# Performance work log

Measured on AMD Instinct MI355X. Metric: run time of the kernel, lower is better.

Reference implementation:

```python
import jax, jax.numpy as jnp
import numpy as np

D = 768
NH = 8
HD = D // NH
LAT = 64


def layernorm(x, g, b, eps=1e-5):
    mu = x.mean(-1, keepdims=True)
    var = ((x - mu) ** 2).mean(-1, keepdims=True)
    return (x - mu) * jax.lax.rsqrt(var + eps) * g + b


def mha(q, k, v, qw, qb, kw, kb, vw, vb, ow, ob):
    # torch nn.MultiheadAttention (batch_first): Linear is x @ W.T + b
    B, Lq, _ = q.shape
    qh = (q @ qw.T + qb).reshape(B, Lq, NH, HD)
    kh = (k @ kw.T + kb).reshape(B, -1, NH, HD)
    vh = (v @ vw.T + vb).reshape(B, -1, NH, HD)
    s = jnp.einsum('bqhd,bkhd->bhqk', qh, kh) * (1.0 / np.sqrt(HD))
    a = jax.nn.softmax(s, axis=-1)
    o = jnp.einsum('bhqk,bkhd->bqhd', a, vh).reshape(B, Lq, D)
    return o @ ow.T + ob


def setup_inputs() -> dict:
    key = jax.random.key(0)
    ks = jax.random.split(key, 16)
    w = lambda k, shape: (jax.random.normal(k, shape, jnp.float32) * 0.02)
    inp = {
        'frames': jax.random.normal(ks[0], (4, 4, 8, 3, 224, 224), jnp.float32),
        'pe_w': w(ks[1], (D, 3, 14, 14)), 'pe_b': jnp.zeros((D,), jnp.float32),
        'latents': jax.random.normal(ks[2], (LAT, D), jnp.float32),
        'ca_qw': w(ks[3], (D, D)), 'ca_qb': jnp.zeros((D,), jnp.float32),
        'ca_kw': w(ks[4], (D, D)), 'ca_kb': jnp.zeros((D,), jnp.float32),
        'ca_vw': w(ks[5], (D, D)), 'ca_vb': jnp.zeros((D,), jnp.float32),
        'ca_ow': w(ks[6], (D, D)), 'ca_ob': jnp.zeros((D,), jnp.float32),
        'nq_g': jnp.ones((D,), jnp.float32), 'nq_b': jnp.zeros((D,), jnp.float32),
        'nkv_g': jnp.ones((D,), jnp.float32), 'nkv_b': jnp.zeros((D,), jnp.float32),
        'no_g': jnp.ones((D,), jnp.float32), 'no_b': jnp.zeros((D,), jnp.float32),
        'm1_w': w(ks[7], (4 * D, D)), 'm1_b': jnp.zeros((4 * D,), jnp.float32),
        'm2_w': w(ks[8], (D, 4 * D)), 'm2_b': jnp.zeros((D,), jnp.float32),
        'sa_qw': w(ks[9], (D, D)), 'sa_qb': jnp.zeros((D,), jnp.float32),
        'sa_kw': w(ks[10], (D, D)), 'sa_kb': jnp.zeros((D,), jnp.float32),
        'sa_vw': w(ks[11], (D, D)), 'sa_vb': jnp.zeros((D,), jnp.float32),
        'sa_ow': w(ks[12], (D, D)), 'sa_ob': jnp.zeros((D,), jnp.float32),
        'f1_w': w(ks[13], (2 * D, D)), 'f1_b': jnp.zeros((2 * D,), jnp.float32),
        'f2_w': w(ks[14], (D, 2 * D)), 'f2_b': jnp.zeros((D,), jnp.float32),
        'n1_g': jnp.ones((D,), jnp.float32), 'n1_b': jnp.zeros((D,), jnp.float32),
        'n2_g': jnp.ones((D,), jnp.float32), 'n2_b': jnp.zeros((D,), jnp.float32),
    }
    return inp


def reference(frames, pe_w, pe_b, latents, ca_qw, ca_qb, ca_kw, ca_kb, ca_vw, ca_vb,
              ca_ow, ca_ob, nq_g, nq_b, nkv_g, nkv_b, no_g, no_b, m1_w, m1_b, m2_w, m2_b,
              sa_qw, sa_qb, sa_kw, sa_kb, sa_vw, sa_vb, sa_ow, sa_ob, f1_w, f1_b,
              f2_w, f2_b, n1_g, n1_b, n2_g, n2_b):
    B, S, T, C, H, W = frames.shape
    # --- patch embed (Conv2d k=14 s=14), batched over all seconds & frames ---
    f = frames.reshape(B * S * T, C, H, W)
    p = jax.lax.conv_general_dilated(
        f, pe_w, window_strides=(14, 14), padding='VALID',
        dimension_numbers=('NCHW', 'OIHW', 'NCHW')) + pe_b[None, :, None, None]
    npatch = p.shape[2] * p.shape[3]  # 256 patches per frame
    p = p.reshape(B * S * T, D, npatch).transpose(0, 2, 1)  # [BST, P, D]
    kv = p.reshape(B * S, T * npatch, D)  # per-second patch tokens
    # --- Perceiver second tokenizer (loop over seconds == batched over B*S) ---
    q = jnp.broadcast_to(latents[None], (B * S, LAT, D))
    out = mha(layernorm(q, nq_g, nq_b), layernorm(kv, nkv_g, nkv_b), kv,
              ca_qw, ca_qb, ca_kw, ca_kb, ca_vw, ca_vb, ca_ow, ca_ob)
    h = layernorm(out, no_g, no_b)
    tok = out + (jax.nn.gelu(h @ m1_w.T + m1_b) @ m2_w.T + m2_b)
    # concat second tokens along time
    x = tok.reshape(B, S * LAT, D)
    # --- temporal_agg: TransformerEncoderLayer (post-norm, relu, eval mode) ---
    attn = mha(x, x, x, sa_qw, sa_qb, sa_kw, sa_kb, sa_vw, sa_vb, sa_ow, sa_ob)
    x = layernorm(x + attn, n1_g, n1_b)
    ff = jax.nn.relu(x @ f1_w.T + f1_b) @ f2_w.T + f2_b
    x = layernorm(x + ff, n2_g, n2_b)
    return x
```

## Files before the change

### kernel.cpp

```cpp
#include <hip/hip_runtime.h>
#include <hip/hip_bf16.h>
#include <math.h>

typedef __hip_bfloat16 bf16;
typedef __attribute__((ext_vector_type(8))) short short8;
typedef __attribute__((ext_vector_type(4))) short short4v;
typedef __attribute__((ext_vector_type(4))) float f32x4;

__device__ __forceinline__ void gload16(const bf16* g, bf16* l) {
  __builtin_amdgcn_global_load_lds((const __attribute__((address_space(1))) void*)(g),
                                   (__attribute__((address_space(3))) void*)(l), 16, 0, 0);
}
__device__ __forceinline__ float bfu2f(unsigned short u) {
  union { unsigned u; float f; } c; c.u = ((unsigned)u) << 16; return c.f;
}
__device__ __forceinline__ short bf2s(float v) {
  union { bf16 h; short s; } c; c.h = __float2bfloat16(v); return c.s;
}
__device__ __forceinline__ short4v packbf4(f32x4 v) {
  short4v o;
  o[0] = bf2s(v[0]); o[1] = bf2s(v[1]); o[2] = bf2s(v[2]); o[3] = bf2s(v[3]);
  return o;
}

struct Seg { const float* src; bf16* dst; int rows, sc, dc; const float* scale; };
struct Segs { Seg s[13]; };

__global__ __launch_bounds__(256) void preproc_kernel(
    Segs segs,
    const float* __restrict__ frames, bf16* __restrict__ imcol,
    const float* __restrict__ kw, const float* __restrict__ nkv_g,
    const float* __restrict__ nkv_b, const float* __restrict__ kb,
    float* __restrict__ s1, float* __restrict__ s2,
    const float* __restrict__ latents, const float* __restrict__ nq_g,
    const float* __restrict__ nq_b, bf16* __restrict__ q_ln,
    const float* __restrict__ ba, const float* __restrict__ bb,
    const float* __restrict__ bc, float* __restrict__ sab_cat) {
  __shared__ float red[16];
  int b = blockIdx.x, tid = threadIdx.x;
  if (b < 29952) {
    Seg sg = segs.s[b / 2304];
    int bx = b % 2304;
    long long total = (long long)sg.rows * sg.dc;
    for (long long idx = (long long)bx * 256 + tid; idx < total; idx += 2304LL * 256) {
      int r = (int)(idx / sg.dc), c = (int)(idx % sg.dc);
      float v = (c < sg.sc) ? sg.src[(long long)r * sg.sc + c] : 0.f;
      if (sg.scale && c < sg.sc) v *= sg.scale[c];
      sg.dst[idx] = __float2bfloat16(v);
    }
  } else if (b < 40192) {
    unsigned idx8 = (unsigned)(b - 29952) * 256u + tid;
    unsigned m = idx8 / 80u;
    unsigned k0 = (idx8 % 80u) * 8u;
    unsigned n = m >> 8;
    unsigned p = m & 255u;
    unsigned py = p >> 4, px = p & 15u;
    const float* fb = frames + ((size_t)n * 3u) * 224u * 224u +
                      (size_t)py * 14u * 224u + px * 14u;
    short8 o;
    #pragma unroll
    for (int e = 0; e < 8; ++e) {
      unsigned k = k0 + e;
      float v = 0.f;
      if (k < 588u) {
        unsigned c = k / 196u, r = k % 196u;
        unsigned i = r / 14u, j = r % 14u;
        v = fb[((size_t)c * 224u + i) * 224u + j];
      }
      o[e] = bf2s(v);
    }
    *(short8*)(imcol + (size_t)m * 640u + k0) = o;
  } else if (b < 40960) {
    int j = b - 40192;
    const float* wr_ = kw + (size_t)j * 768;
    float a = 0.f, c = 0.f;
    #pragma unroll
    for (int i = 0; i < 3; ++i) {
      int d = tid + i * 256;
      float wv = wr_[d];
      a += wv * nkv_g[d];
      c += wv * nkv_b[d];
    }
    for (int off = 32; off; off >>= 1) { a += __shfl_down(a, off); c += __shfl_down(c, off); }
    int w = tid >> 6;
    if ((tid & 63) == 0) { red[w] = a; red[8 + w] = c; }
    __syncthreads();
    if (tid == 0) {
      s1[j] = red[0] + red[1] + red[2] + red[3];
      s2[j] = red[8] + red[9] + red[10] + red[11] + kb[j];
    }
  } else if (b < 41088) {
    int row = b - 40960;
    size_t base = (size_t)row * 768;
    if (row >= 64) {
      for (int i = 0; i < 3; ++i) q_ln[base + tid + i * 256] = __float2bfloat16(0.f);
      return;
    }
    float x[3];
    for (int i = 0; i < 3; ++i) x[i] = latents[base + tid + i * 256];
    float s = x[0] + x[1] + x[2];
    float sq = x[0] * x[0] + x[1] * x[1] + x[2] * x[2];
    for (int off = 32; off; off >>= 1) {
      s += __shfl_down(s, off);
      sq += __shfl_down(sq, off);
    }
    int w = tid >> 6;
    if ((tid & 63) == 0) { red[w] = s; red[4 + w] = sq; }
    __syncthreads();
    if (tid == 0) {
      red[0] = red[0] + red[1] + red[2] + red[3];
      red[4] = red[4] + red[5] + red[6] + red[7];
    }
    __syncthreads();
    float mean = red[0] * (1.f / 768.f);
    float var = red[4] * (1.f / 768.f) - mean * mean;
    float rs = rsqrtf(var + 1e-5f);
    for (int i = 0; i < 3; ++i) {
      int c = tid + i * 256;
      q_ln[base + c] = __float2bfloat16((x[i] - mean) * rs * nq_g[c] + nq_b[c]);
    }
  } else {
    int i = (b - 41088) * 256 + tid;
    if (i < 2304)
      sab_cat[i] = i < 768 ? ba[i] : (i < 1536 ? bb[i - 768] : bc[i - 1536]);
  }
}

__global__ __launch_bounds__(256) void rowstats_kernel(const bf16* __restrict__ x,
                                                       float* __restrict__ mu,
                                                       float* __restrict__ rs) {
  int row = blockIdx.x * 4 + (threadIdx.x >> 6);
  int lane = threadIdx.x & 63;
  const unsigned short* p = (const unsigned short*)(x + (size_t)row * 768);
  float s = 0.f, sq = 0.f;
  #pragma unroll
  for (int i = 0; i < 3; ++i) {
    ushort4 v = *(const ushort4*)(p + lane * 4 + i * 256);
    float f0 = bfu2f(v.x), f1 = bfu2f(v.y), f2 = bfu2f(v.z), f3 = bfu2f(v.w);
    s += f0 + f1 + f2 + f3;
    sq += f0 * f0 + f1 * f1 + f2 * f2 + f3 * f3;
  }
  for (int off = 32; off; off >>= 1) { s += __shfl_down(s, off); sq += __shfl_down(sq, off); }
  if (lane == 0) {
    float m = s * (1.f / 768.f);
    float var = sq * (1.f / 768.f) - m * m;
    mu[row] = m;
    rs[row] = rsqrtf(var + 1e-5f);
  }
}

__global__ __launch_bounds__(256) void ln_kernel(const float* __restrict__ inF,
                                                 const bf16* __restrict__ inB,
                                                 const float* __restrict__ g,
                                                 const float* __restrict__ b,
                                                 float* __restrict__ outF,
                                                 bf16* __restrict__ outB,
                                                 int validRows) {
  int row = blockIdx.x;
  int tid = threadIdx.x;
  __shared__ float red[8];
  size_t base = (size_t)row * 768;
  if (row >= validRows) {
    for (int i = 0; i < 3; ++i) {
      int c = tid + i * 256;
      if (outB) outB[base + c] = __float2bfloat16(0.f);
      if (outF) outF[base + c] = 0.f;
    }
    return;
  }
  float x[3];
  for (int i = 0; i < 3; ++i) {
    int c = tid + i * 256;
    x[i] = inF ? inF[base + c] : __bfloat162float(inB[base + c]);
  }
  float s = x[0] + x[1] + x[2];
  float sq = x[0] * x[0] + x[1] * x[1] + x[2] * x[2];
  for (int off = 32; off; off >>= 1) {
    s += __shfl_down(s, off);
    sq += __shfl_down(sq, off);
  }
  int w = tid >> 6;
  if ((tid & 63) == 0) { red[w] = s; red[4 + w] = sq; }
  __syncthreads();
  if (tid == 0) {
    red[0] = red[0] + red[1] + red[2] + red[3];
    red[4] = red[4] + red[5] + red[6] + red[7];
  }
  __syncthreads();
  float mean = red[0] * (1.f / 768.f);
  float var = red[4] * (1.f / 768.f) - mean * mean;
  float rs = rsqrtf(var + 1e-5f);
  for (int i = 0; i < 3; ++i) {
    int c = tid + i * 256;
    float y = (x[i] - mean) * rs * g[c] + b[c];
    if (outF) outF[base + c] = y;
    if (outB) outB[base + c] = __float2bfloat16(y);
  }
}

__global__ __launch_bounds__(512, 2) void gemm256(
    const bf16* __restrict__ A, const bf16* __restrict__ Bw,
    const float* __restrict__ bias,
    bf16* __restrict__ outB,
    int M, int N, int K, int act,
    const float* __restrict__ rowMu, const float* __restrict__ rowRs,
    const float* __restrict__ s1, const float* __restrict__ s2,
    bf16* __restrict__ outB2) {
  __shared__ __align__(16) bf16 As[2][8192];
  __shared__ __align__(16) bf16 Bs[2][8192];
  int tid = threadIdx.x;
  int nwg = gridDim.x * gridDim.y;
  int orig = blockIdx.y * gridDim.x + blockIdx.x;
  int xcd = orig & 7, loc = orig >> 3;
  int qq = nwg >> 3, rr = nwg & 7;
  int swz = (xcd < rr) ? (xcd * (qq + 1) + loc) : (rr * (qq + 1) + (xcd - rr) * qq + loc);
  int m0 = (swz / gridDim.x) * 256, n0 = (swz % gridDim.x) * 256;

  int lane = tid & 63, w = tid >> 6;
  int wr = w >> 2, wc = w & 3;
  int l15 = lane & 15, lq = lane >> 4;

  f32x4 acc[8][4] = {};

  #define STAGE256(buf, kt)                                                     \
    {                                                                           \
      _Pragma("unroll")                                                         \
      for (int i = 0; i < 2; ++i) {                                             \
        int r = w * 2 + i;                                                      \
        int koct = r >> 2, row = (r & 3) * 64 + lane;                           \
        gload16(A + (size_t)(m0 + row) * K + (kt) + koct * 8,                   \
                &As[buf][r * 512]);                                             \
        gload16(Bw + (size_t)(n0 + row) * K + (kt) + koct * 8,                  \
                &Bs[buf][r * 512]);                                             \
      }                                                                         \
    }

  int nt = K >> 5;
  STAGE256(0, 0);
  for (int t = 0; t < nt; ++t) {
    int cur = t & 1;
    if (t + 1 < nt) {
      STAGE256(cur ^ 1, (t + 1) << 5);
      asm volatile("s_waitcnt vmcnt(4)" ::: "memory");
    } else {
      asm volatile("s_waitcnt vmcnt(0)" ::: "memory");
    }
    __builtin_amdgcn_s_barrier();
    asm volatile("" ::: "memory");
    short8 af[8], bfr[4];
    #pragma unroll
    for (int mi = 0; mi < 8; ++mi)
      af[mi] = *(const short8*)(&As[cur][(lq * 256 + wr * 128 + mi * 16 + l15) * 8]);
    #pragma unroll
    for (int ni = 0; ni < 4; ++ni)
      bfr[ni] = *(const short8*)(&Bs[cur][(lq * 256 + wc * 64 + ni * 16 + l15) * 8]);
    __builtin_amdgcn_s_setprio(1);
    #pragma unroll
    for (int mi = 0; mi < 8; ++mi)
      #pragma unroll
      for (int ni = 0; ni < 4; ++ni)
        acc[mi][ni] = __builtin_amdgcn_mfma_f32_16x16x32_bf16(bfr[ni], af[mi],
                                                              acc[mi][ni], 0, 0, 0);
    __builtin_amdgcn_s_setprio(0);
    asm volatile("" ::: "memory");
    __builtin_amdgcn_s_barrier();
  }
  #undef STAGE256

  bf16* ldsflat = (bf16*)As;
  bf16* ep = ldsflat + w * 1152;
  int rlo = lane >> 3, cg = lane & 7;

  if (act == 3) {
    int c0w = n0 + wc * 64;
    bool isV = (c0w < 768);
    bf16* dst = isV ? outB : outB2;
    int colbase = isV ? c0w : (c0w - 768);
    f32x4 bv[4], a1[4], a2[4];
    #pragma unroll
    for (int ni = 0; ni < 4; ++ni) {
      int cc = colbase + ni * 16 + lq * 4;
      if (isV) bv[ni] = *(const f32x4*)(bias + cc);
      else { a1[ni] = *(const f32x4*)(s1 + cc); a2[ni] = *(const f32x4*)(s2 + cc); }
    }
    #pragma unroll
    for (int mi = 0; mi < 8; ++mi) {
      int roww = m0 + wr * 128 + mi * 16 + l15;
      float rs_ = 0.f, mu_ = 0.f;
      if (!isV) { rs_ = rowRs[roww]; mu_ = rowMu[roww]; }
      #pragma unroll
      for (int ni = 0; ni < 4; ++ni) {
        f32x4 v;
        if (isV) v = acc[mi][ni] + bv[ni];
        else {
          #pragma unroll
          for (int j = 0; j < 4; ++j)
            v[j] = rs_ * (acc[mi][ni][j] - mu_ * a1[ni][j]) + a2[ni][j];
        }
        *(short4v*)(ep + l15 * 72 + ni * 16 + lq * 4) = packbf4(v);
      }
      asm volatile("s_waitcnt lgkmcnt(0)" ::: "memory");
      #pragma unroll
      for (int p = 0; p < 2; ++p) {
        int r = p * 8 + rlo;
        short8 d = *(const short8*)(ep + r * 72 + cg * 8);
        int rg = m0 + wr * 128 + mi * 16 + r;
        *(short8*)(dst + (size_t)rg * 768 + colbase + cg * 8) = d;
      }
      asm volatile("s_waitcnt lgkmcnt(0)" ::: "memory");
    }
    return;
  }

  {
    int c0w = n0 + wc * 64;
    f32x4 bv[4] = {};
    if (bias) {
      #pragma unroll
      for (int ni = 0; ni < 4; ++ni)
        bv[ni] = *(const f32x4*)(bias + c0w + ni * 16 + lq * 4);
    }
    #pragma unroll
    for (int mi = 0; mi < 8; ++mi) {
      #pragma unroll
      for (int ni = 0; ni < 4; ++ni) {
        f32x4 v = acc[mi][ni] + bv[ni];
        *(short4v*)(ep + l15 * 72 + ni * 16 + lq * 4) = packbf4(v);
      }
      asm volatile("s_waitcnt lgkmcnt(0)" ::: "memory");
      #pragma unroll
      for (int p = 0; p < 2; ++p) {
        int r = p * 8 + rlo;
        short8 d = *(const short8*)(ep + r * 72 + cg * 8);
        int rg = m0 + wr * 128 + mi * 16 + r;
        *(short8*)(outB + (size_t)rg * N + c0w + cg * 8) = d;
      }
      asm volatile("s_waitcnt lgkmcnt(0)" ::: "memory");
    }
  }
}

__global__ __launch_bounds__(256) void gemm_bf16(
    const bf16* __restrict__ A, const bf16* __restrict__ Bw,
    const float* __restrict__ bias, const float* __restrict__ resid,
    float* __restrict__ outF, bf16* __restrict__ outB,
    int M, int N, int K, int act) {
  __shared__ __align__(16) bf16 As[2][4096];
  __shared__ __align__(16) bf16 Bs[2][4096];
  int tid = threadIdx.x;
  int nwg = gridDim.x * gridDim.y;
  int orig = blockIdx.y * gridDim.x + blockIdx.x;
  int xcd = orig & 7, loc = orig >> 3;
  int qq = nwg >> 3, rr = nwg & 7;
  int swz = (xcd < rr) ? (xcd * (qq + 1) + loc) : (rr * (qq + 1) + (xcd - rr) * qq + loc);
  int m0 = (swz / gridDim.x) * 128, n0 = (swz % gridDim.x) * 128;

  int lane = tid & 63, w = tid >> 6;
  int wr = w >> 1, wc = w & 1;
  int l15 = lane & 15, lq = lane >> 4;
  const bf16* Abase = A + (size_t)m0 * K + w * 8;
  const bf16* Bbase = Bw + (size_t)n0 * K + w * 8;
  f32x4 acc[4][4] = {};

  int nt = K >> 5;
  #pragma unroll
  for (int i = 0; i < 2; ++i) {
    int r = i * 64 + lane;
    gload16(Abase + (size_t)r * K, &As[0][(w * 2 + i) * 512]);
    gload16(Bbase + (size_t)r * K, &Bs[0][(w * 2 + i) * 512]);
  }
  for (int t = 0; t < nt; ++t) {
    int cur = t & 1;
    if (t + 1 < nt) {
      int kt = (t + 1) << 5;
      #pragma unroll
      for (int i = 0; i < 2; ++i) {
        int r = i * 64 + lane;
        gload16(Abase + (size_t)r * K + kt, &As[cur ^ 1][(w * 2 + i) * 512]);
        gload16(Bbase + (size_t)r * K + kt, &Bs[cur ^ 1][(w * 2 + i) * 512]);
      }
      asm volatile("s_waitcnt vmcnt(4)" ::: "memory");
    } else {
      asm volatile("s_waitcnt vmcnt(0)" ::: "memory");
    }
    __builtin_amdgcn_s_barrier();
    asm volatile("" ::: "memory");
    const bf16* Ab = &As[cur][lq * 1024];
    const bf16* Bb = &Bs[cur][lq * 1024];
    short8 af[4], bfr[4];
    #pragma unroll
    for (int mi = 0; mi < 4; ++mi)
      af[mi] = *(const short8*)(Ab + (wr * 64 + mi * 16 + l15) * 8);
    #pragma unroll
    for (int ni = 0; ni < 4; ++ni)
      bfr[ni] = *(const short8*)(Bb + (wc * 64 + ni * 16 + l15) * 8);
    __builtin_amdgcn_s_setprio(1);
    #pragma unroll
    for (int mi = 0; mi < 4; ++mi)
      #pragma unroll
      for (int ni = 0; ni < 4; ++ni)
        acc[mi][ni] = __builtin_amdgcn_mfma_f32_16x16x32_bf16(bfr[ni], af[mi],
                                                              acc[mi][ni], 0, 0, 0);
    __builtin_amdgcn_s_setprio(0);
    asm volatile("" ::: "memory");
    __builtin_amdgcn_s_barrier();
  }

  #pragma unroll
  for (int ni = 0; ni < 4; ++ni) {
    int c0 = n0 + wc * 64 + ni * 16 + lq * 4;
    f32x4 bv = {};
    if (bias) bv = *(const f32x4*)(bias + c0);
    #pragma unroll
    for (int mi = 0; mi < 4; ++mi) {
      int row = m0 + wr * 64 + mi * 16 + l15;
      f32x4 v = acc[mi][ni] + bv;
      if (act == 1) {
        #pragma unroll
        for (int j = 0; j < 4; ++j) {
          float x = v[j];
          v[j] = 0.5f * x * (1.f + tanhf(0.79788456080286535f * (x + 0.044715f * x * x * x)));
        }
      } else if (act == 2) {
        #pragma unroll
        for (int j = 0; j < 4; ++j) v[j] = fmaxf(v[j], 0.f);
      }
      size_t idx = (size_t)row * N + c0;
      if (resid) v += *(const f32x4*)(resid + idx);
      if (outF) *(f32x4*)(outF + idx) = v;
      if (outB) *(short4v*)(outB + idx) = packbf4(v);
    }
  }
}

__global__ __launch_bounds__(256) void flash_kernel(
    const bf16* __restrict__ Q, const bf16* __restrict__ Kp,
    const bf16* __restrict__ V, bf16* __restrict__ O,
    int Lk, int qRPB, int kRPB, int oRPB, int ld) {
  const float scale = 0.10206207261596575f;
  __shared__ bf16 Vt[96 * 72];
  __shared__ bf16 Ps[4 * 16 * 72];
  int tid = threadIdx.x, lane = tid & 63, w = tid >> 6;
  int l15 = lane & 15, lq = lane >> 4;
  int b = blockIdx.z, h = blockIdx.y, qt = blockIdx.x;
  int qbase = b * qRPB + qt * 64 + w * 16;
  int kbase = b * kRPB;
  int obase = b * oRPB + qt * 64 + w * 16;
  int ch = h * 96;

  short8 aQ[3];
  #pragma unroll
  for (int kd = 0; kd < 3; ++kd)
    aQ[kd] = *(const short8*)(Q + (size_t)(qbase + l15) * ld + ch + kd * 32 + lq * 8);

  f32x4 oacc[6] = {};
  float mrun[4] = {-1e30f, -1e30f, -1e30f, -1e30f};
  float lrun[4] = {0.f, 0.f, 0.f, 0.f};

  for (int kc = 0; kc < Lk; kc += 64) {
    for (int u = tid; u < 768; u += 256) {
      int kk = u / 12, dc = u % 12;
      short8 v = *(const short8*)(V + (size_t)(kbase + kc + kk) * ld + ch + dc * 8);
      const bf16* pv = (const bf16*)&v;
      #pragma unroll
      for (int e = 0; e < 8; ++e) Vt[(dc * 8 + e) * 72 + kk] = pv[e];
    }
    __syncthreads();

    f32x4 sacc[4] = {};
    #pragma unroll
    for (int ni = 0; ni < 4; ++ni)
      #pragma unroll
      for (int kd = 0; kd < 3; ++kd) {
        short8 bK = *(const short8*)(Kp + (size_t)(kbase + kc + ni * 16 + l15) * ld +
                                     ch + kd * 32 + lq * 8);
        sacc[ni] = __builtin_amdgcn_mfma_f32_16x16x32_bf16(aQ[kd], bK, sacc[ni], 0, 0, 0);
      }
    #pragma unroll
    for (int ni = 0; ni < 4; ++ni)
      #pragma unroll
      for (int j = 0; j < 4; ++j) sacc[ni][j] *= scale;

    float al[4];
    #pragma unroll
    for (int j = 0; j < 4; ++j) {
      float mx = fmaxf(fmaxf(sacc[0][j], sacc[1][j]), fmaxf(sacc[2][j], sacc[3][j]));
      #pragma unroll
      for (int off = 1; off < 16; off <<= 1) mx = fmaxf(mx, __shfl_xor(mx, off));
      float mnew = fmaxf(mrun[j], mx);
      float alpha = __expf(mrun[j] - mnew);
      float rsum = 0.f;
      #pragma unroll
      for (int ni = 0; ni < 4; ++ni) {
        float p = __expf(sacc[ni][j] - mnew);
        sacc[ni][j] = p;
        rsum += p;
      }
      #pragma unroll
      for (int off = 1; off < 16; off <<= 1) rsum += __shfl_xor(rsum, off);
      lrun[j] = lrun[j] * alpha + rsum;
      mrun[j] = mnew;
      al[j] = alpha;
    }

    #pragma unroll
    for (int ni = 0; ni < 4; ++ni)
      #pragma unroll
      for (int j = 0; j < 4; ++j)
        Ps[(w * 16 + lq * 4 + j) * 72 + ni * 16 + l15] = __float2bfloat16(sacc[ni][j]);
    #pragma unroll
    for (int t = 0; t < 6; ++t)
      #pragma unroll
      for (int j = 0; j < 4; ++j) oacc[t][j] *= al[j];
    short8 aP[2];
    #pragma unroll
    for (int ks = 0; ks < 2; ++ks)
      aP[ks] = *(const short8*)(&Ps[(w * 16 + l15) * 72 + ks * 32 + lq * 8]);
    #pragma unroll
    for (int t = 0; t < 6; ++t)
      #pragma unroll
      for (int ks = 0; ks < 2; ++ks) {
        short8 bV = *(const short8*)(&Vt[(t * 16 + l15) * 72 + ks * 32 + lq * 8]);
        oacc[t] = __builtin_amdgcn_mfma_f32_16x16x32_bf16(aP[ks], bV, oacc[t], 0, 0, 0);
      }
    __syncthreads();
  }

  #pragma unroll
  for (int t = 0; t < 6; ++t)
    #pragma unroll
    for (int j = 0; j < 4; ++j) {
      int row = obase + lq * 4 + j;
      int col = ch + t * 16 + l15;
      O[(size_t)row * 768 + col] = __float2bfloat16(oacc[t][j] / lrun[j]);
    }
}

__global__ __launch_bounds__(256) void flash_split_kernel(
    const bf16* __restrict__ Q, const bf16* __restrict__ Kp,
    const bf16* __restrict__ V, float* __restrict__ Opart,
    float* __restrict__ Mpart, float* __restrict__ Lpart,
    int splitLen, int kRPB) {
  const float scale = 0.10206207261596575f;
  __shared__ bf16 Vt[96 * 72];
  __shared__ bf16 Ps[4 * 16 * 72];
  int tid = threadIdx.x, lane = tid & 63, w = tid >> 6;
  int l15 = lane & 15, lq = lane >> 4;
  int s = blockIdx.x, h = blockIdx.y, b = blockIdx.z;
  int kbase = b * kRPB + s * splitLen;
  int ch = h * 96;

  short8 aQ[3];
  #pragma unroll
  for (int kd = 0; kd < 3; ++kd)
    aQ[kd] = *(const short8*)(Q + (size_t)(w * 16 + l15) * 768 + ch + kd * 32 + lq * 8);

  f32x4 oacc[6] = {};
  float mrun[4] = {-1e30f, -1e30f, -1e30f, -1e30f};
  float lrun[4] = {0.f, 0.f, 0.f, 0.f};

  for (int kc = 0; kc < splitLen; kc += 64) {
    for (int u = tid; u < 768; u += 256) {
      int kk = u / 12, dc = u % 12;
      short8 v = *(const short8*)(V + (size_t)(kbase + kc + kk) * 768 + ch + dc * 8);
      const bf16* pv = (const bf16*)&v;
      #pragma unroll
      for (int e = 0; e < 8; ++e) Vt[(dc * 8 + e) * 72 + kk] = pv[e];
    }
    __syncthreads();

    f32x4 sacc[4] = {};
    #pragma unroll
    for (int ni = 0; ni < 4; ++ni)
      #pragma unroll
      for (int kd = 0; kd < 3; ++kd) {
        short8 bK = *(const short8*)(Kp + (size_t)(kbase + kc + ni * 16 + l15) * 768 +
                                     ch + kd * 32 + lq * 8);
        sacc[ni] = __builtin_amdgcn_mfma_f32_16x16x32_bf16(aQ[kd], bK, sacc[ni], 0, 0, 0);
      }
    #pragma unroll
    for (int ni = 0; ni < 4; ++ni)
      #pragma unroll
      for (int j = 0; j < 4; ++j) sacc[ni][j] *= scale;

    float al[4];
    #pragma unroll
    for (int j = 0; j < 4; ++j) {
      float mx = fmaxf(fmaxf(sacc[0][j], sacc[1][j]), fmaxf(sacc[2][j], sacc[3][j]));
      #pragma unroll
      for (int off = 1; off < 16; off <<= 1) mx = fmaxf(mx, __shfl_xor(mx, off));
      float mnew = fmaxf(mrun[j], mx);
      float alpha = __expf(mrun[j] - mnew);
      float rsum = 0.f;
      #pragma unroll
      for (int ni = 0; ni < 4; ++ni) {
        float p = __expf(sacc[ni][j] - mnew);
        sacc[ni][j] = p;
        rsum += p;
      }
      #pragma unroll
      for (int off = 1; off < 16; off <<= 1) rsum += __shfl_xor(rsum, off);
      lrun[j] = lrun[j] * alpha + rsum;
      mrun[j] = mnew;
      al[j] = alpha;
    }

    #pragma unroll
    for (int ni = 0; ni < 4; ++ni)
      #pragma unroll
      for (int j = 0; j < 4; ++j)
        Ps[(w * 16 + lq * 4 + j) * 72 + ni * 16 + l15] = __float2bfloat16(sacc[ni][j]);
    #pragma unroll
    for (int t = 0; t < 6; ++t)
      #pragma unroll
      for (int j = 0; j < 4; ++j) oacc[t][j] *= al[j];
    short8 aP[2];
    #pragma unroll
    for (int ks = 0; ks < 2; ++ks)
      aP[ks] = *(const short8*)(&Ps[(w * 16 + l15) * 72 + ks * 32 + lq * 8]);
    #pragma unroll
    for (int t = 0; t < 6; ++t)
      #pragma unroll
      for (int ks = 0; ks < 2; ++ks) {
        short8 bV = *(const short8*)(&Vt[(t * 16 + l15) * 72 + ks * 32 + lq * 8]);
        oacc[t] = __builtin_amdgcn_mfma_f32_16x16x32_bf16(aP[ks], bV, oacc[t], 0, 0, 0);
      }
    __syncthreads();
  }

  int orow = b * 64 + w * 16;
  #pragma unroll
  for (int t = 0; t < 6; ++t)
    #pragma unroll
    for (int j = 0; j < 4; ++j)
      Opart[(size_t)(s * 1024 + orow + lq * 4 + j) * 768 + ch + t * 16 + l15] = oacc[t][j];
  if (l15 == 0) {
    #pragma unroll
    for (int j = 0; j < 4; ++j) {
      int qqi = w * 16 + lq * 4 + j;
      int mi = ((s * 16 + b) * 8 + h) * 64 + qqi;
      Mpart[mi] = mrun[j];
      Lpart[mi] = lrun[j];
    }
  }
}

__global__ __launch_bounds__(256) void flash_merge_kernel(
    const float* __restrict__ Opart, const float* __restrict__ Mpart,
    const float* __restrict__ Lpart, bf16* __restrict__ O, int nsplit) {
  int row = blockIdx.x;
  int tid = threadIdx.x;
  int c0 = tid * 3;
  int b = row >> 6, q = row & 63;
  int h = c0 / 96;
  float m = -1e30f;
  for (int s = 0; s < nsplit; ++s)
    m = fmaxf(m, Mpart[((s * 16 + b) * 8 + h) * 64 + q]);
  float l = 0.f, o0 = 0.f, o1 = 0.f, o2 = 0.f;
  for (int s = 0; s < nsplit; ++s) {
    int mi = ((s * 16 + b) * 8 + h) * 64 + q;
    float ws = __expf(Mpart[mi] - m);
    l += ws * Lpart[mi];
    const float* op = Opart + (size_t)(s * 1024 + row) * 768 + c0;
    o0 += ws * op[0]; o1 += ws * op[1]; o2 += ws * op[2];
  }
  float inv = 1.f / l;
  size_t ob = (size_t)row * 768 + c0;
  O[ob]     = __float2bfloat16(o0 * inv);
  O[ob + 1] = __float2bfloat16(o1 * inv);
  O[ob + 2] = __float2bfloat16(o2 * inv);
}

extern "C" void kernel_launch(void* const* d_in, const int* in_sizes, int n_in,
                              void* d_out, int out_size, void* d_ws, size_t ws_size,
                              hipStream_t stream) {
  const float* frames = (const float*)d_in[0];
  const float* pe_w   = (const float*)d_in[1];
  const float* pe_b   = (const float*)d_in[2];
  const float* latents= (const float*)d_in[3];
  const float* ca_qw  = (const float*)d_in[4];  const float* ca_qb = (const float*)d_in[5];
  const float* ca_kw  = (const float*)d_in[6];  const float* ca_kb = (const float*)d_in[7];
  const float* ca_vw  = (const float*)d_in[8];  const float* ca_vb = (const float*)d_in[9];
  const float* ca_ow  = (const float*)d_in[10]; const float* ca_ob = (const float*)d_in[11];
  const float* nq_g   = (const float*)d_in[12]; const float* nq_b  = (const float*)d_in[13];
  const float* nkv_g  = (const float*)d_in[14]; const float* nkv_b = (const float*)d_in[15];
  const float* no_g   = (const float*)d_in[16]; const float* no_b  = (const float*)d_in[17];
  const float* m1_w   = (const float*)d_in[18]; const float* m1_b  = (const float*)d_in[19];
  const float* m2_w   = (const float*)d_in[20]; const float* m2_b  = (const float*)d_in[21];
  const float* sa_qw  = (const float*)d_in[22]; const float* sa_qb = (const float*)d_in[23];
  const float* sa_kw  = (const float*)d_in[24]; const float* sa_kb = (const float*)d_in[25];
  const float* sa_vw  = (const float*)d_in[26]; const float* sa_vb = (const float*)d_in[27];
  const float* sa_ow  = (const float*)d_in[28]; const float* sa_ob = (const float*)d_in[29];
  const float* f1_w   = (const float*)d_in[30]; const float* f1_b  = (const float*)d_in[31];
  const float* f2_w   = (const float*)d_in[32]; const float* f2_b  = (const float*)d_in[33];
  const float* n1_g   = (const float*)d_in[34]; const float* n1_b  = (const float*)d_in[35];
  const float* n2_g   = (const float*)d_in[36]; const float* n2_b  = (const float*)d_in[37];

  char* ws = (char*)d_ws;
  size_t off = 0;
  auto take = [&](size_t bytes) -> char* {
    char* p = ws + off;
    off += (bytes + 255) & ~(size_t)255;
    return p;
  };

  bf16* w_pe   = (bf16*)take((size_t)768 * 640 * 2);
  bf16* w_caq  = (bf16*)take((size_t)768 * 768 * 2);
  bf16* w_cakv = (bf16*)take((size_t)1536 * 768 * 2);
  bf16* w_cao  = (bf16*)take((size_t)768 * 768 * 2);
  bf16* w_m1   = (bf16*)take((size_t)3072 * 768 * 2);
  bf16* w_m2   = (bf16*)take((size_t)768 * 3072 * 2);
  bf16* w_saq  = (bf16*)take((size_t)768 * 768 * 2);
  bf16* w_sak  = (bf16*)take((size_t)768 * 768 * 2);
  bf16* w_sav  = (bf16*)take((size_t)768 * 768 * 2);
  bf16* w_sao  = (bf16*)take((size_t)768 * 768 * 2);
  bf16* w_f1   = (bf16*)take((size_t)1536 * 768 * 2);
  bf16* w_f2   = (bf16*)take((size_t)768 * 1536 * 2);
  float* sab_cat = (float*)take((size_t)2304 * 4);
  float* s1v  = (float*)take((size_t)768 * 4);
  float* s2v  = (float*)take((size_t)768 * 4);
  float* muv  = (float*)take((size_t)32768 * 4);
  float* rsv  = (float*)take((size_t)32768 * 4);

  bf16* q_ln = (bf16*)take((size_t)128 * 768 * 2);
  bf16* qh   = (bf16*)take((size_t)128 * 768 * 2);

  bf16* kv   = (bf16*)take((size_t)32768 * 768 * 2);
  bf16* vhkh = (bf16*)take((size_t)2 * 32768 * 768 * 2);
  bf16* vh = vhkh;
  bf16* kh = vhkh + (size_t)32768 * 768;
  bf16* imcol = vhkh;

  const size_t REGION = (size_t)32768 * 608 * 2;
  char* region = take(REGION);
  float* Opart = (float*)region;
  float* Mpart = (float*)(region + 25165824);
  float* Lpart = (float*)(region + 25165824 + 262144);
  bf16*  attn_o = (bf16*)(region + REGION - (size_t)1024 * 768 * 2);
  size_t ro = 0;
  auto rtake = [&](size_t bytes) -> char* {
    char* p = region + ro;
    ro += (bytes + 255) & ~(size_t)255;
    return p;
  };
  float* out_f  = (float*)rtake((size_t)1024 * 768 * 4);
  bf16*  h_b    = (bf16*)rtake((size_t)1024 * 768 * 2);
  bf16*  g_b    = (bf16*)rtake((size_t)1024 * 3072 * 2);
  float* tok_f  = (float*)rtake((size_t)1024 * 768 * 4);
  bf16*  tok_b  = (bf16*)rtake((size_t)1024 * 768 * 2);
  bf16*  xqkv   = (bf16*)rtake((size_t)1024 * 2304 * 2);
  bf16*  sa_o   = (bf16*)rtake((size_t)1024 * 768 * 2);
  float* y_f    = (float*)rtake((size_t)1024 * 768 * 4);
  float* x1f    = (float*)rtake((size_t)1024 * 768 * 4);
  bf16*  x1b    = (bf16*)rtake((size_t)1024 * 768 * 2);
  bf16*  ff1    = (bf16*)rtake((size_t)1024 * 1536 * 2);
  float* z_f    = (float*)rtake((size_t)1024 * 768 * 4);
  (void)ws_size; (void)in_sizes; (void)n_in; (void)out_size;

  Segs segs;
  segs.s[0]  = {pe_w,  w_pe,  768, 588, 640, nullptr};
  segs.s[1]  = {ca_qw, w_caq, 768, 768, 768, nullptr};
  segs.s[2]  = {ca_vw, w_cakv, 768, 768, 768, nullptr};
  segs.s[3]  = {ca_kw, w_cakv + (size_t)768 * 768, 768, 768, 768, nkv_g};
  segs.s[4]  = {ca_ow, w_cao, 768, 768, 768, nullptr};
  segs.s[5]  = {m1_w,  w_m1,  3072, 768, 768, nullptr};
  segs.s[6]  = {m2_w,  w_m2,  768, 3072, 3072, nullptr};
  segs.s[7]  = {sa_qw, w_saq, 768, 768, 768, nullptr};
  segs.s[8]  = {sa_kw, w_sak, 768, 768, 768, nullptr};
  segs.s[9]  = {sa_vw, w_sav, 768, 768, 768, nullptr};
  segs.s[10] = {f1_w,  w_f1,  1536, 768, 768, nullptr};
  segs.s[11] = {f2_w,  w_f2,  768, 1536, 1536, nullptr};
  segs.s[12] = {sa_ow, w_sao, 768, 768, 768, nullptr};
  preproc_kernel<<<41097, 256, 0, stream>>>(
      segs, frames, imcol,
      ca_kw, nkv_g, nkv_b, ca_kb, s1v, s2v,
      latents, nq_g, nq_b, q_ln,
      sa_qb, sa_kb, sa_vb, sab_cat);

  gemm256<<<dim3(3, 128), 512, 0, stream>>>(imcol, w_pe, pe_b, kv,
                                            32768, 768, 640, 0,
                                            nullptr, nullptr, nullptr, nullptr, nullptr);

  gemm_bf16<<<dim3(6, 1), 256, 0, stream>>>(q_ln, w_caq, ca_qb, nullptr, nullptr, qh,
                                            128, 768, 768, 0);

  rowstats_kernel<<<8192, 256, 0, stream>>>(kv, muv, rsv);

  gemm256<<<dim3(6, 128), 512, 0, stream>>>(kv, w_cakv, ca_vb, vh,
                                            32768, 1536, 768, 3,
                                            muv, rsv, s1v, s2v, kh);

  flash_split_kernel<<<dim3(8, 8, 16), 256, 0, stream>>>(qh, kh, vh, Opart, Mpart, Lpart,
                                                         256, 2048);
  flash_merge_kernel<<<1024, 256, 0, stream>>>(Opart, Mpart, Lpart, attn_o, 8);

  gemm_bf16<<<dim3(6, 8), 256, 0, stream>>>(attn_o, w_cao, ca_ob, nullptr, out_f, nullptr,
                                            1024, 768, 768, 0);

  ln_kernel<<<1024, 256, 0, stream>>>(out_f, nullptr, no_g, no_b, nullptr, h_b, 1024);

  gemm_bf16<<<dim3(24, 8), 256, 0, stream>>>(h_b, w_m1, m1_b, nullptr, nullptr, g_b,
                                             1024, 3072, 768, 1);

  gemm_bf16<<<dim3(6, 8), 256, 0, stream>>>(g_b, w_m2, m2_b, out_f, tok_f, tok_b,
                                            1024, 768, 3072, 0);

  gemm_bf16<<<dim3(18, 8), 256, 0, stream>>>(tok_b, w_saq, sab_cat, nullptr, nullptr, xqkv,
                                             1024, 2304, 768, 0);

  flash_kernel<<<dim3(4, 8, 4), 256, 0, stream>>>(xqkv, xqkv + 768, xqkv + 1536, sa_o,
                                                  256, 256, 256, 256, 2304);

  gemm_bf16<<<dim3(6, 8), 256, 0, stream>>>(sa_o, w_sao, sa_ob, tok_f, y_f, nullptr,
                                            1024, 768, 768, 0);

  ln_kernel<<<1024, 256, 0, stream>>>(y_f, nullptr, n1_g, n1_b, x1f, x1b, 1024);

  gemm_bf16<<<dim3(12, 8), 256, 0, stream>>>(x1b, w_f1, f1_b, nullptr, nullptr, ff1,
                                             1024, 1536, 768, 2);

  gemm_bf16<<<dim3(6, 8), 256, 0, stream>>>(ff1, w_f2, f2_b, x1f, z_f, nullptr,
                                            1024, 768, 1536, 0);

  ln_kernel<<<1024, 256, 0, stream>>>(z_f, nullptr, n2_g, n2_b, (float*)d_out, nullptr, 1024);
}
```

Measured before the change: 716.4 us.

## Deepen gemm256 pipeline to four LDS buffers with half-tile interleaved loads

The 256x256 GEMM main loop moves from a double-buffered LDS ring to a four-buffer ring that prefetches two to three K-tiles ahead. Each iteration is split into two half-M MFMA phases, and the global-to-LDS loads for future tiles are interleaved between those phases under finer vmcnt waits. The goal is to hide global memory latency and lower fragment register pressure, since only 4 A fragments are live at a time. In exchange the kernel uses twice the LDS (128 KB per block), which may conflict with the launch bound of 2 blocks per CU, and it adds extra barriers per iteration.

```diff
diff --git a/kernel.cpp b/kernel.cpp
--- a/kernel.cpp
+++ b/kernel.cpp
@@ -206,8 +206,8 @@
     const float* __restrict__ rowMu, const float* __restrict__ rowRs,
     const float* __restrict__ s1, const float* __restrict__ s2,
     bf16* __restrict__ outB2) {
-  __shared__ __align__(16) bf16 As[2][8192];
-  __shared__ __align__(16) bf16 Bs[2][8192];
+  __shared__ __align__(16) bf16 As[4][8192];
+  __shared__ __align__(16) bf16 Bs[4][8192];
   int tid = threadIdx.x;
   int nwg = gridDim.x * gridDim.y;
   int orig = blockIdx.y * gridDim.x + blockIdx.x;
@@ -222,41 +222,44 @@
 
   f32x4 acc[8][4] = {};
 
-  #define STAGE256(buf, kt)                                                     \
-    {                                                                           \
-      _Pragma("unroll")                                                         \
-      for (int i = 0; i < 2; ++i) {                                             \
-        int r = w * 2 + i;                                                      \
-        int koct = r >> 2, row = (r & 3) * 64 + lane;                           \
-        gload16(A + (size_t)(m0 + row) * K + (kt) + koct * 8,                   \
-                &As[buf][r * 512]);                                             \
-        gload16(Bw + (size_t)(n0 + row) * K + (kt) + koct * 8,                  \
-                &Bs[buf][r * 512]);                                             \
-      }                                                                         \
-    }
-
-  int nt = K >> 5;
-  STAGE256(0, 0);
-  for (int t = 0; t < nt; ++t) {
-    int cur = t & 1;
-    if (t + 1 < nt) {
-      STAGE256(cur ^ 1, (t + 1) << 5);
-      asm volatile("s_waitcnt vmcnt(4)" ::: "memory");
-    } else {
-      asm volatile("s_waitcnt vmcnt(0)" ::: "memory");
-    }
+  #define STAGEH(buf, kt, part)                                                \
+    {                                                                          \
+      int koct_ = w >> 1;                                                      \
+      int row0_ = (w & 1) * 64 + ((part) & 1) * 128;                           \
+      if ((part) < 2)                                                          \
+        gload16(A + (size_t)(m0 + row0_ + lane) * K + (kt) + koct_ * 8,        \
+                &As[buf][(koct_ * 256 + row0_) * 8]);                          \
+      else                                                                     \
+        gload16(Bw + (size_t)(n0 + row0_ + lane) * K + (kt) + koct_ * 8,       \
+                &Bs[buf][(koct_ * 256 + row0_) * 8]);                          \
+    }
+
+  int T = K >> 5;
+  #pragma unroll
+  for (int p = 0; p < 4; ++p) STAGEH(0, 0, p);
+  #pragma unroll
+  for (int p = 0; p < 4; ++p) STAGEH(1, 32, p);
+  STAGEH(2, 64, 0);
+  STAGEH(2, 64, 1);
+  asm volatile("s_waitcnt vmcnt(6)" ::: "memory");
+  __builtin_amdgcn_s_barrier();
+
+  for (int t = 0; t < T; ++t) {
+    int bufc = t & 3, bufn2 = (t + 2) & 3, bufn3 = (t + 3) & 3;
+    int kt2 = (t + 2) << 5, kt3 = (t + 3) << 5;
+    short8 af[4], bfr[4];
+    #pragma unroll
+    for (int ni = 0; ni < 4; ++ni)
+      bfr[ni] = *(const short8*)(&Bs[bufc][(lq * 256 + wc * 64 + ni * 16 + l15) * 8]);
+    #pragma unroll
+    for (int mi = 0; mi < 4; ++mi)
+      af[mi] = *(const short8*)(&As[bufc][(lq * 256 + wr * 128 + mi * 16 + l15) * 8]);
+    if (t + 2 < T) { STAGEH(bufn2, kt2, 2); STAGEH(bufn2, kt2, 3); }
     __builtin_amdgcn_s_barrier();
     asm volatile("" ::: "memory");
-    short8 af[8], bfr[4];
-    #pragma unroll
-    for (int mi = 0; mi < 8; ++mi)
-      af[mi] = *(const short8*)(&As[cur][(lq * 256 + wr * 128 + mi * 16 + l15) * 8]);
-    #pragma unroll
-    for (int ni = 0; ni < 4; ++ni)
-      bfr[ni] = *(const short8*)(&Bs[cur][(lq * 256 + wc * 64 + ni * 16 + l15) * 8]);
     __builtin_amdgcn_s_setprio(1);
     #pragma unroll
-    for (int mi = 0; mi < 8; ++mi)
+    for (int mi = 0; mi < 4; ++mi)
       #pragma unroll
       for (int ni = 0; ni < 4; ++ni)
         acc[mi][ni] = __builtin_amdgcn_mfma_f32_16x16x32_bf16(bfr[ni], af[mi],
@@ -264,8 +267,31 @@
     __builtin_amdgcn_s_setprio(0);
     asm volatile("" ::: "memory");
     __builtin_amdgcn_s_barrier();
-  }
-  #undef STAGE256
+    #pragma unroll
+    for (int mi = 0; mi < 4; ++mi)
+      af[mi] = *(const short8*)(&As[bufc][(lq * 256 + wr * 128 + 64 + mi * 16 + l15) * 8]);
+    if (t + 3 < T) { STAGEH(bufn3, kt3, 0); STAGEH(bufn3, kt3, 1); }
+    if (t + 3 < T) {
+      asm volatile("s_waitcnt vmcnt(6)" ::: "memory");
+    } else if (t + 2 < T) {
+      asm volatile("s_waitcnt vmcnt(4)" ::: "memory");
+    } else if (t + 1 < T) {
+      asm volatile("s_waitcnt vmcnt(0)" ::: "memory");
+    }
+    __builtin_amdgcn_s_barrier();
+    asm volatile("" ::: "memory");
+    __builtin_amdgcn_s_setprio(1);
+    #pragma unroll
+    for (int mi = 0; mi < 4; ++mi)
+      #pragma unroll
+      for (int ni = 0; ni < 4; ++ni)
+        acc[4 + mi][ni] = __builtin_amdgcn_mfma_f32_16x16x32_bf16(bfr[ni], af[mi],
+                                                                  acc[4 + mi][ni], 0, 0, 0);
+    __builtin_amdgcn_s_setprio(0);
+    asm volatile("" ::: "memory");
+    __builtin_amdgcn_s_barrier();
+  }
+  #undef STAGEH
 
   bf16* ldsflat = (bf16*)As;
   bf16* ep = ldsflat + w * 1152;
```

Measured after the change: 676.5 us (median of 3 runs). 1.06x faster.

## Double GEMM K-tile to 64 and interleave next-tile loads with MFMA

Applied to the files above, without the earlier changes.

The bf16 GEMM now stages a 64-deep K tile per iteration instead of 32, which doubles the shared-memory buffers for A and B and halves the number of loop iterations and barriers. The global-to-LDS loads for the next tile are split into eight pieces. Two pieces are issued up front and the rest are spread between the four sub-blocks of MFMA work, so memory traffic overlaps with compute. The cost is a much larger LDS footprint per block (about 128 KB), which likely allows only one resident 512-thread block per CU despite the launch bound of two.

```diff
diff --git a/kernel.cpp b/kernel.cpp
--- a/kernel.cpp
+++ b/kernel.cpp
@@ -206,8 +206,8 @@
     const float* __restrict__ rowMu, const float* __restrict__ rowRs,
     const float* __restrict__ s1, const float* __restrict__ s2,
     bf16* __restrict__ outB2) {
-  __shared__ __align__(16) bf16 As[2][8192];
-  __shared__ __align__(16) bf16 Bs[2][8192];
+  __shared__ __align__(16) bf16 As[2][16384];
+  __shared__ __align__(16) bf16 Bs[2][16384];
   int tid = threadIdx.x;
   int nwg = gridDim.x * gridDim.y;
   int orig = blockIdx.y * gridDim.x + blockIdx.x;
@@ -222,50 +222,66 @@
 
   f32x4 acc[8][4] = {};
 
-  #define STAGE256(buf, kt)                                                     \
-    {                                                                           \
-      _Pragma("unroll")                                                         \
-      for (int i = 0; i < 2; ++i) {                                             \
-        int r = w * 2 + i;                                                      \
-        int koct = r >> 2, row = (r & 3) * 64 + lane;                           \
-        gload16(A + (size_t)(m0 + row) * K + (kt) + koct * 8,                   \
-                &As[buf][r * 512]);                                             \
-        gload16(Bw + (size_t)(n0 + row) * K + (kt) + koct * 8,                  \
-                &Bs[buf][r * 512]);                                             \
-      }                                                                         \
-    }
-
-  int nt = K >> 5;
-  STAGE256(0, 0);
-  for (int t = 0; t < nt; ++t) {
-    int cur = t & 1;
-    if (t + 1 < nt) {
-      STAGE256(cur ^ 1, (t + 1) << 5);
-      asm volatile("s_waitcnt vmcnt(4)" ::: "memory");
+  #define STAGEQ(buf, kt, p)                                                   \
+    {                                                                          \
+      int rowq_ = ((p) & 3) * 64 + lane;                                       \
+      if ((p) < 4)                                                             \
+        gload16(A + (size_t)(m0 + rowq_) * K + (kt) + w * 8,                   \
+                &As[buf][(w * 256 + ((p) & 3) * 64) * 8]);                     \
+      else                                                                     \
+        gload16(Bw + (size_t)(n0 + rowq_) * K + (kt) + w * 8,                  \
+                &Bs[buf][(w * 256 + ((p) & 3) * 64) * 8]);                     \
+    }
+
+  int T = K >> 6;
+  #pragma unroll
+  for (int p = 0; p < 8; ++p) STAGEQ(0, 0, p);
+
+  for (int t = 0; t < T; ++t) {
+    int cur = t & 1, nxt = cur ^ 1;
+    int ktn = (t + 1) << 6;
+    __builtin_amdgcn_s_barrier();
+    if (t + 1 < T) {
+      STAGEQ(nxt, ktn, 0);
+      STAGEQ(nxt, ktn, 1);
+      asm volatile("s_waitcnt vmcnt(2)" ::: "memory");
     } else {
       asm volatile("s_waitcnt vmcnt(0)" ::: "memory");
     }
     __builtin_amdgcn_s_barrier();
     asm volatile("" ::: "memory");
-    short8 af[8], bfr[4];
-    #pragma unroll
-    for (int mi = 0; mi < 8; ++mi)
-      af[mi] = *(const short8*)(&As[cur][(lq * 256 + wr * 128 + mi * 16 + l15) * 8]);
-    #pragma unroll
-    for (int ni = 0; ni < 4; ++ni)
-      bfr[ni] = *(const short8*)(&Bs[cur][(lq * 256 + wc * 64 + ni * 16 + l15) * 8]);
-    __builtin_amdgcn_s_setprio(1);
-    #pragma unroll
-    for (int mi = 0; mi < 8; ++mi)
+    #pragma unroll
+    for (int kh = 0; kh < 2; ++kh) {
+      short8 bfr[4];
       #pragma unroll
       for (int ni = 0; ni < 4; ++ni)
-        acc[mi][ni] = __builtin_amdgcn_mfma_f32_16x16x32_bf16(bfr[ni], af[mi],
-                                                              acc[mi][ni], 0, 0, 0);
-    __builtin_amdgcn_s_setprio(0);
-    asm volatile("" ::: "memory");
-    __builtin_amdgcn_s_barrier();
-  }
-  #undef STAGE256
+        bfr[ni] = *(const short8*)(
+            &Bs[cur][((kh * 4 + lq) * 256 + wc * 64 + ni * 16 + l15) * 8]);
+      #pragma unroll
+      for (int mh = 0; mh < 2; ++mh) {
+        short8 af[4];
+        #pragma unroll
+        for (int mi = 0; mi < 4; ++mi)
+          af[mi] = *(const short8*)(
+              &As[cur][((kh * 4 + lq) * 256 + wr * 128 + mh * 64 + mi * 16 + l15) * 8]);
+        if (t + 1 < T) {
+          int pp = (kh * 2 + mh) * 2 + 2;
+          if (pp < 8) { STAGEQ(nxt, ktn, pp); STAGEQ(nxt, ktn, pp + 1); }
+        }
+        __builtin_amdgcn_s_setprio(1);
+        #pragma unroll
+        for (int mi = 0; mi < 4; ++mi)
+          #pragma unroll
+          for (int ni = 0; ni < 4; ++ni)
+            acc[mh * 4 + mi][ni] = __builtin_amdgcn_mfma_f32_16x16x32_bf16(
+                bfr[ni], af[mi], acc[mh * 4 + mi][ni], 0, 0, 0);
+        __builtin_amdgcn_s_setprio(0);
+        asm volatile("" ::: "memory");
+      }
+    }
+  }
+  #undef STAGEQ
+  __builtin_amdgcn_s_barrier();
 
   bf16* ldsflat = (bf16*)As;
   bf16* ep = ldsflat + w * 1152;
```

Result: faster. 686.1 us (-4.2%).
